# Performance work log

Measured on AMD Instinct MI355X. Metric: run time of the kernel, lower is better.

The kernel has to match this reference:

```python
import jax, jax.numpy as jnp
import numpy as np

B, T, C, H, K = 4, 2048, 1024, 16, 64
CHUNK = 64
NUM_LAYERS, LAYER_ID = 12, 6
D_MIX, D_DECAY = 32, 64


def setup_inputs() -> dict:
    key = jax.random.key(0)
    ks = jax.random.split(key, 12)
    x = jax.random.normal(ks[0], (B, T, C), jnp.float32)
    shift_state_in = jax.random.normal(ks[1], (B, C), jnp.float32)
    wkv_state_in = jnp.zeros((B, H, K, K), jnp.float32)

    r01 = LAYER_ID / max(NUM_LAYERS - 1, 1)
    r10 = 1.0 - LAYER_ID / NUM_LAYERS
    ddd = (np.arange(C, dtype=np.float64) / C)
    maa = lambda p: jnp.asarray((1.0 - ddd ** p).reshape(1, 1, C), jnp.float32)
    time_maa_x = maa(r10)
    time_maa_w = maa(r10)
    time_maa_k = maa(r10)
    time_maa_v = jnp.asarray((1.0 - (ddd ** r10 + 0.3 * r01)).reshape(1, 1, C), jnp.float32)
    time_maa_r = maa(0.5 * r10)
    time_maa_g = maa(0.5 * r10)
    time_maa_w1 = jax.random.uniform(ks[2], (C, D_MIX * 5), jnp.float32, -0.01, 0.01)
    time_maa_w2 = jax.random.uniform(ks[3], (5, D_MIX, C), jnp.float32, -0.01, 0.01)

    n = np.arange(C, dtype=np.float64)
    time_decay = jnp.asarray((-6 + 5 * (n / (C - 1)) ** (0.7 + 1.3 * r01)).reshape(1, 1, C), jnp.float32)
    time_decay_w1 = jax.random.uniform(ks[4], (C, D_DECAY), jnp.float32, -0.01, 0.01)
    time_decay_w2 = jax.random.uniform(ks[5], (D_DECAY, C), jnp.float32, -0.01, 0.01)

    zig = ((n + 1) % 3 - 1) * 0.1
    time_faaaa = jnp.asarray((r01 * (1 - n / (C - 1)) + zig).reshape(H, K), jnp.float32)
    lucid_temperature = jnp.ones((1, H, 1, 1), jnp.float32)

    s = 0.02
    W_r = jax.random.normal(ks[6], (C, C), jnp.float32) * s
    W_k = jax.random.normal(ks[7], (C, C), jnp.float32) * s
    W_v = jax.random.normal(ks[8], (C, C), jnp.float32) * s
    W_g = jax.random.normal(ks[9], (C, C), jnp.float32) * s
    W_o = jax.random.normal(ks[10], (C, C), jnp.float32) * s
    ln_gamma = jnp.ones((C,), jnp.float32)
    ln_beta = jnp.zeros((C,), jnp.float32)

    return dict(x=x, shift_state_in=shift_state_in, wkv_state_in=wkv_state_in,
                time_maa_x=time_maa_x, time_maa_w=time_maa_w, time_maa_k=time_maa_k,
                time_maa_v=time_maa_v, time_maa_r=time_maa_r, time_maa_g=time_maa_g,
                time_maa_w1=time_maa_w1, time_maa_w2=time_maa_w2,
                time_decay=time_decay, time_decay_w1=time_decay_w1, time_decay_w2=time_decay_w2,
                time_faaaa=time_faaaa, lucid_temperature=lucid_temperature,
                W_r=W_r, W_k=W_k, W_v=W_v, W_g=W_g, W_o=W_o,
                ln_gamma=ln_gamma, ln_beta=ln_beta)


def _forward(x, shift_state_in, wkv_state_in, time_maa_x, time_maa_w, time_maa_k,
             time_maa_v, time_maa_r, time_maa_g, time_maa_w1, time_maa_w2,
             time_decay, time_decay_w1, time_decay_w2, time_faaaa, lucid_temperature,
             W_r, W_k, W_v, W_g, W_o, ln_gamma, ln_beta):
    # ddlerp token shift
    dxprev = jnp.concatenate([shift_state_in[:, None, :], x[:, :-1]], axis=1) - x
    xxx = jnp.tanh((x + dxprev * time_maa_x) @ time_maa_w1).reshape(B, T, 5, D_MIX)
    m = jnp.einsum('btfd,fdc->fbtc', xxx, time_maa_w2)  # (5,B,T,C)
    mw, mk, mv, mr, mg = m[0], m[1], m[2], m[3], m[4]
    xw = x + dxprev * (time_maa_w + mw)
    xk = x + dxprev * (time_maa_k + mk)
    xv = x + dxprev * (time_maa_v + mv)
    xr = x + dxprev * (time_maa_r + mr)
    xg = x + dxprev * (time_maa_g + mg)

    r = xr @ W_r.T
    k = xk @ W_k.T
    v = xv @ W_v.T
    g = jax.nn.silu(xg @ W_g.T)
    w = time_decay + jnp.tanh(xw @ time_decay_w1) @ time_decay_w2

    tohead = lambda a: a.reshape(B, T, H, K).transpose(0, 2, 1, 3)  # (B,H,T,K)
    r_h, k_h, v_h = tohead(r), tohead(k), tohead(v)
    w_h = -jnp.exp(tohead(w))  # log-decay, negative
    u = time_faaaa.reshape(1, H, 1, K)
    temp = jax.nn.softplus(lucid_temperature)  # (1,H,1,1)

    n_chunks = T // CHUNK
    tochunks = lambda a: a.reshape(B, H, n_chunks, CHUNK, K).transpose(2, 0, 1, 3, 4)
    eye = jnp.eye(CHUNK, dtype=jnp.float32)
    mid = CHUNK // 2

    def step(state, inp):
        r_c, k_c, v_c, w_log = inp  # each (B,H,cs,K)
        w_cum = jnp.cumsum(w_log, axis=-2)
        w_shift = jnp.pad(w_cum[..., :-1, :], ((0, 0), (0, 0), (1, 0), (0, 0)))
        offset = w_shift[..., mid:mid + 1, :]
        r_decay = jnp.exp(jnp.clip(w_shift - offset, -30, 30))
        k_inv_decay = jnp.exp(jnp.clip(offset - w_cum, -30, 30))
        A = jnp.einsum('bhtk,bhsk->bhts', r_c * r_decay, k_c * k_inv_decay)
        A = jnp.tril(A, -1) + eye * jnp.sum(r_c * (u * k_c), axis=-1)[..., None]
        k_norm = k_c / jnp.maximum(jnp.linalg.norm(k_c, axis=-1, keepdims=True), 1e-12)
        K_gram = jnp.einsum('bhtk,bhsk->bhts', k_norm, k_norm)
        P = eye + jnp.exp(jnp.clip(temp * K_gram, -20, 20))
        P_v = jnp.linalg.solve(P, v_c)
        w_intra = jnp.exp(jnp.clip(w_cum - w_log, -30, 30))
        y = A @ P_v + (r_c * w_intra) @ state
        w_sum = jnp.sum(w_log, axis=-2, keepdims=True)  # (B,H,1,K)
        w_inter = jnp.exp(jnp.clip(w_sum - w_cum, -30, 30))
        new_state = state * jnp.exp(w_sum) + jnp.einsum('bhtk,bhtv->bhkv', k_c * w_inter, v_c)
        return new_state, y

    state_out, ys = jax.lax.scan(
        step, wkv_state_in,
        (tochunks(r_h), tochunks(k_h), tochunks(v_h), tochunks(w_h)))
    # (n,B,H,cs,K) -> (B,T,C)
    y = ys.transpose(1, 2, 0, 3, 4).reshape(B, H, T, K).transpose(0, 2, 1, 3).reshape(B, T, C)

    # GroupNorm with n_head groups, eps = 1e-5 * head_size_divisor**2
    eps = 1e-5 * 64.0
    yg = y.reshape(B, T, H, K)
    mu = yg.mean(axis=-1, keepdims=True)
    var = yg.var(axis=-1, keepdims=True)
    yn = (yg - mu) / jnp.sqrt(var + eps)
    yn = yn * ln_gamma.reshape(1, 1, H, K) + ln_beta.reshape(1, 1, H, K)
    yn = yn.reshape(B, T, C)

    out = (yn * g) @ W_o.T
    return out, x[:, -1], state_out


def reference(x, shift_state_in, wkv_state_in, time_maa_x, time_maa_w, time_maa_k,
              time_maa_v, time_maa_r, time_maa_g, time_maa_w1, time_maa_w2,
              time_decay, time_decay_w1, time_decay_w2, time_faaaa, lucid_temperature,
              W_r, W_k, W_v, W_g, W_o, ln_gamma, ln_beta):
    return _forward(x, shift_state_in, wkv_state_in, time_maa_x, time_maa_w, time_maa_k,
                    time_maa_v, time_maa_r, time_maa_g, time_maa_w1, time_maa_w2,
                    time_decay, time_decay_w1, time_decay_w2, time_faaaa, lucid_temperature,
                    W_r, W_k, W_v, W_g, W_o, ln_gamma, ln_beta)
```

## Files before the change

### kernel.cpp

```cpp
#include <hip/hip_runtime.h>
#include <cstdint>
#include <cstddef>

typedef unsigned short ushort_t;
#define DEVI __device__ __forceinline__

constexpr int Bc = 4, Tc = 2048, Cc = 1024, Hc = 16;
constexpr int BT = Bc * Tc;
constexpr int NCHUNK = Tc / 64;

using f32x4  = __attribute__((ext_vector_type(4))) float;
using bf16x8 = __attribute__((ext_vector_type(8))) __bf16;

DEVI ushort_t f2bf(float f) {
  union { float f; unsigned u; } v; v.f = f;
  unsigned r = v.u + 0x7fffu + ((v.u >> 16) & 1u);
  return (ushort_t)(r >> 16);
}
DEVI float bf2f(ushort_t u) {
  union { unsigned u; float f; } v; v.u = ((unsigned)u) << 16; return v.f;
}
DEVI float clip30(float x) { return fminf(fmaxf(x, -30.f), 30.f); }
DEVI float clip20(float x) { return fminf(fmaxf(x, -20.f), 20.f); }

DEVI float4 bf4up(uint2 r) {
  float4 v;
  v.x = bf2f((ushort_t)(r.x & 0xffff)); v.y = bf2f((ushort_t)(r.x >> 16));
  v.z = bf2f((ushort_t)(r.y & 0xffff)); v.w = bf2f((ushort_t)(r.y >> 16));
  return v;
}
DEVI uint2 f4pk(float4 v) {
  uint2 r;
  r.x = (unsigned)f2bf(v.x) | ((unsigned)f2bf(v.y) << 16);
  r.y = (unsigned)f2bf(v.z) | ((unsigned)f2bf(v.w) << 16);
  return r;
}

DEVI void gload_lds16(const ushort_t* g, ushort_t* l) {
  __builtin_amdgcn_global_load_lds(
      (const __attribute__((address_space(1))) void*)g,
      (__attribute__((address_space(3))) void*)l, 16, 0, 0);
}

#define GETEL(V4, E) ((E) == 0 ? (V4).x : (E) == 1 ? (V4).y : (E) == 2 ? (V4).z : (V4).w)
#define SETEL(V4, E, VAL) do { if ((E) == 0) (V4).x = (VAL); else if ((E) == 1) (V4).y = (VAL); \
                               else if ((E) == 2) (V4).z = (VAL); else (V4).w = (VAL); } while (0)

__global__ void k_f2bf5(const float* __restrict__ i0, const float* __restrict__ i1,
                        const float* __restrict__ i2, const float* __restrict__ i3,
                        const float* __restrict__ i4,
                        ushort_t* __restrict__ o0, ushort_t* __restrict__ o1,
                        ushort_t* __restrict__ o2, ushort_t* __restrict__ o3,
                        ushort_t* __restrict__ o4) {
  int z = blockIdx.z;
  const float* in = (z == 0) ? i0 : (z == 1) ? i1 : (z == 2) ? i2 : (z == 3) ? i3 : i4;
  ushort_t* out   = (z == 0) ? o0 : (z == 1) ? o1 : (z == 2) ? o2 : (z == 3) ? o3 : o4;
  int i = blockIdx.x * 256 + threadIdx.x;
  if (i < Cc * Cc / 4) {
    float4 v = *(const float4*)(in + (size_t)i * 4);
    ushort4 o;
    o.x = f2bf(v.x); o.y = f2bf(v.y); o.z = f2bf(v.z); o.w = f2bf(v.w);
    *(ushort4*)(out + (size_t)i * 4) = o;
  }
}

__global__ void k_prep(const float* __restrict__ w2, const float* __restrict__ w1,
                       const float* __restrict__ dw1, const float* __restrict__ x,
                       ushort_t* __restrict__ w2t, ushort_t* __restrict__ w1t,
                       ushort_t* __restrict__ dw1t, float* __restrict__ xlast) {
  int i = blockIdx.x * 256 + threadIdx.x;
  if (i < 163840) {
    int c = i / 160, fd = i % 160;
    w2t[i] = f2bf(w2[(size_t)fd * 1024 + c]);
  } else if (i < 327680) {
    int j = i - 163840; int n = j >> 10, r = j & 1023;
    w1t[j] = f2bf(w1[(size_t)r * 160 + n]);
  } else if (i < 393216) {
    int j = i - 327680; int n = j >> 10, r = j & 1023;
    dw1t[j] = f2bf(dw1[(size_t)r * 64 + n]);
  } else if (i < 397312) {
    int j = i - 393216; int b = j >> 10, c = j & 1023;
    xlast[j] = x[((size_t)b * Tc + Tc - 1) * Cc + c];
  }
}

__global__ __launch_bounds__(256) void k_shift_tanh(
    const float* __restrict__ x, const float* __restrict__ sst,
    const float* __restrict__ tmx, const ushort_t* __restrict__ Wt,
    ushort_t* __restrict__ outv) {
  constexpr int NCOLS = 160, NF = NCOLS / 16;
  int tid = threadIdx.x;
  int wave = tid >> 6, lane = tid & 63;
  int row0 = (blockIdx.x * 4 + wave) * 16;
  int lr = lane & 15, lk = (lane >> 4) * 8;
  int rg = row0 + lr;
  int tt = rg & (Tc - 1);
  const float* xrow = x + (size_t)rg * Cc;
  const float* prow = (tt == 0) ? (sst + (size_t)(rg >> 11) * Cc) : (xrow - Cc);
  f32x4 acc[NF];
  #pragma unroll
  for (int n = 0; n < NF; ++n) acc[n] = (f32x4){0.f, 0.f, 0.f, 0.f};
  for (int k0 = 0; k0 < 1024; k0 += 32) {
    int c0 = k0 + lk;
    float4 xa = *(const float4*)(xrow + c0), xb = *(const float4*)(xrow + c0 + 4);
    float4 pa = *(const float4*)(prow + c0), pb = *(const float4*)(prow + c0 + 4);
    float4 ta = *(const float4*)(tmx + c0), tb = *(const float4*)(tmx + c0 + 4);
    union { bf16x8 v; uint2 u[2]; } cv;
    cv.u[0] = f4pk(make_float4(xa.x + (pa.x - xa.x) * ta.x, xa.y + (pa.y - xa.y) * ta.y,
                               xa.z + (pa.z - xa.z) * ta.z, xa.w + (pa.w - xa.w) * ta.w));
    cv.u[1] = f4pk(make_float4(xb.x + (pb.x - xb.x) * tb.x, xb.y + (pb.y - xb.y) * tb.y,
                               xb.z + (pb.z - xb.z) * tb.z, xb.w + (pb.w - xb.w) * tb.w));
    #pragma unroll
    for (int n = 0; n < NF; ++n) {
      bf16x8 b = *(const bf16x8*)&Wt[(size_t)(n * 16 + lr) * 1024 + k0 + lk];
      acc[n] = __builtin_amdgcn_mfma_f32_16x16x32_bf16(cv.v, b, acc[n], 0, 0, 0);
    }
  }
  #pragma unroll
  for (int n = 0; n < NF; ++n) {
    #pragma unroll
    for (int q = 0; q < 4; ++q) {
      int row = row0 + (lane >> 4) * 4 + q;
      size_t oi = (size_t)row * NCOLS + n * 16 + lr;
      outv[oi] = f2bf(tanhf(acc[n][q]));
    }
  }
}

template<int NCOLS, int OBF>
__global__ __launch_bounds__(256) void k_tanh_mfma(const ushort_t* __restrict__ A,
                                                   const ushort_t* __restrict__ Wt,
                                                   void* __restrict__ outv) {
  constexpr int NF = NCOLS / 16;
  int tid = threadIdx.x;
  int wave = tid >> 6, lane = tid & 63;
  int row0 = (blockIdx.x * 4 + wave) * 16;
  int lr = lane & 15, lk = (lane >> 4) * 8;
  f32x4 acc[NF];
  #pragma unroll
  for (int n = 0; n < NF; ++n) acc[n] = (f32x4){0.f, 0.f, 0.f, 0.f};
  for (int k0 = 0; k0 < 1024; k0 += 32) {
    bf16x8 a = *(const bf16x8*)&A[(size_t)(row0 + lr) * 1024 + k0 + lk];
    #pragma unroll
    for (int n = 0; n < NF; ++n) {
      bf16x8 b = *(const bf16x8*)&Wt[(size_t)(n * 16 + lr) * 1024 + k0 + lk];
      acc[n] = __builtin_amdgcn_mfma_f32_16x16x32_bf16(a, b, acc[n], 0, 0, 0);
    }
  }
  #pragma unroll
  for (int n = 0; n < NF; ++n) {
    #pragma unroll
    for (int q = 0; q < 4; ++q) {
      int row = row0 + (lane >> 4) * 4 + q;
      size_t oi = (size_t)row * NCOLS + n * 16 + lr;
      float v = tanhf(acc[n][q]);
      if (OBF == 1) ((ushort_t*)outv)[oi] = f2bf(v);
      else          ((float*)outv)[oi] = v;
    }
  }
}

__global__ __launch_bounds__(256) void k_mix5m(
    const float* __restrict__ x, const float* __restrict__ sst,
    const ushort_t* __restrict__ t160b, const ushort_t* __restrict__ w2t,
    const float* __restrict__ maaw, const float* __restrict__ maak,
    const float* __restrict__ maav, const float* __restrict__ maar,
    const float* __restrict__ maag,
    ushort_t* __restrict__ xw, ushort_t* __restrict__ xk, ushort_t* __restrict__ xv,
    ushort_t* __restrict__ xr, ushort_t* __restrict__ xg) {
  __shared__ __align__(16) ushort_t As[64 * 168];
  __shared__ __align__(16) ushort_t Bs[64 * 168];
  int tid = threadIdx.x;
  int lane = tid & 63;
  int bRow = blockIdx.x * 64, bCol = blockIdx.y * 64;
  #pragma unroll
  for (int i = 0; i < 5; ++i) {
    int e = tid + i * 256;
    int r = e / 20, cc = (e % 20) * 8;
    *(int4*)&As[r * 168 + cc] = *(const int4*)&t160b[(size_t)(bRow + r) * 160 + cc];
    *(int4*)&Bs[r * 168 + cc] = *(const int4*)&w2t[(size_t)(bCol + r) * 160 + cc];
  }
  __syncthreads();
  int wm = tid >> 7, wn = (tid >> 6) & 1;
  f32x4 acc[5][2][2];
  #pragma unroll
  for (int f = 0; f < 5; ++f)
    #pragma unroll
    for (int m = 0; m < 2; ++m)
      #pragma unroll
      for (int n = 0; n < 2; ++n) acc[f][m][n] = (f32x4){0.f, 0.f, 0.f, 0.f};
  #pragma unroll
  for (int f = 0; f < 5; ++f) {
    bf16x8 af[2], bfv[2];
    #pragma unroll
    for (int m = 0; m < 2; ++m)
      af[m] = *(const bf16x8*)&As[(wm * 32 + m * 16 + (lane & 15)) * 168 + f * 32 + (lane >> 4) * 8];
    #pragma unroll
    for (int n = 0; n < 2; ++n)
      bfv[n] = *(const bf16x8*)&Bs[(wn * 32 + n * 16 + (lane & 15)) * 168 + f * 32 + (lane >> 4) * 8];
    #pragma unroll
    for (int m = 0; m < 2; ++m)
      #pragma unroll
      for (int n = 0; n < 2; ++n)
        acc[f][m][n] = __builtin_amdgcn_mfma_f32_16x16x32_bf16(af[m], bfv[n], acc[f][m][n], 0, 0, 0);
  }
  #pragma unroll
  for (int n = 0; n < 2; ++n) {
    int col = bCol + wn * 32 + n * 16 + (lane & 15);
    float mw_c = maaw[col], mk_c = maak[col], mv_c = maav[col];
    float mr_c = maar[col], mg_c = maag[col];
    #pragma unroll
    for (int m = 0; m < 2; ++m) {
      int row0 = bRow + wm * 32 + m * 16 + (lane >> 4) * 4;
      #pragma unroll
      for (int q = 0; q < 4; ++q) {
        int rg = row0 + q;
        int tt = rg & (Tc - 1);
        size_t g = (size_t)rg * Cc + col;
        float xv0 = x[g];
        float xprev = (tt == 0) ? sst[(size_t)(rg >> 11) * Cc + col] : x[g - Cc];
        float dv = xprev - xv0;
        xw[g] = f2bf(xv0 + dv * (mw_c + acc[0][m][n][q]));
        xk[g] = f2bf(xv0 + dv * (mk_c + acc[1][m][n][q]));
        xv[g] = f2bf(xv0 + dv * (mv_c + acc[2][m][n][q]));
        xr[g] = f2bf(xv0 + dv * (mr_c + acc[3][m][n][q]));
        xg[g] = f2bf(xv0 + dv * (mg_c + acc[4][m][n][q]));
      }
    }
  }
}

template<int EPI, int OBF>
DEVI void gemm_body(const ushort_t* __restrict__ A, const ushort_t* __restrict__ Wt,
                    void* __restrict__ outv, ushort_t* As, ushort_t* Bs,
                    int bRow, int bCol) {
  int tid = threadIdx.x;
  int wave = tid >> 6, lane = tid & 63;
  int wm = wave >> 1, wn = wave & 1;
  int lr = lane >> 2;
  int lkb = (((lane & 3) ^ ((lane >> 3) & 3))) * 8;
  int pch = ((lane >> 4) ^ ((lane >> 1) & 3)) * 8;
  f32x4 zero4 = {0.f, 0.f, 0.f, 0.f};
  f32x4 acc[4][4];
  #pragma unroll
  for (int m = 0; m < 4; ++m)
    #pragma unroll
    for (int n = 0; n < 4; ++n) acc[m][n] = zero4;

#define STAGEK(OFS, K0) do { \
    _Pragma("unroll") \
    for (int i = 0; i < 2; ++i) { \
      int row = (wave + 4 * i) * 16 + lr; \
      gload_lds16(A + (size_t)(bRow + row) * 1024 + (K0) + lkb, &As[(OFS) + (wave + 4 * i) * 512]); \
      gload_lds16(Wt + (size_t)(bCol + row) * 1024 + (K0) + lkb, &Bs[(OFS) + (wave + 4 * i) * 512]); \
    } } while (0)
#define CMP(OFS) do { \
    bf16x8 af[4], bfv[4]; \
    _Pragma("unroll") \
    for (int m = 0; m < 4; ++m) \
      af[m] = *(const bf16x8*)&As[(OFS) + (wm * 64 + m * 16 + (lane & 15)) * 32 + pch]; \
    _Pragma("unroll") \
    for (int n = 0; n < 4; ++n) \
      bfv[n] = *(const bf16x8*)&Bs[(OFS) + (wn * 64 + n * 16 + (lane & 15)) * 32 + pch]; \
    _Pragma("unroll") \
    for (int m = 0; m < 4; ++m) \
      _Pragma("unroll") \
      for (int n = 0; n < 4; ++n) \
        acc[m][n] = __builtin_amdgcn_mfma_f32_16x16x32_bf16(af[m], bfv[n], acc[m][n], 0, 0, 0); \
  } while (0)

  for (int k0 = 0; k0 < 1024; k0 += 64) {
    STAGEK(0, k0);
    STAGEK(4096, k0 + 32);
    __syncthreads();
    CMP(0);
    CMP(4096);
    __syncthreads();
  }
#undef STAGEK
#undef CMP

  #pragma unroll
  for (int m = 0; m < 4; ++m) {
    int row = bRow + wm * 64 + m * 16 + (lane >> 4) * 4;
    #pragma unroll
    for (int n = 0; n < 4; ++n) {
      int col = bCol + wn * 64 + n * 16 + (lane & 15);
      #pragma unroll
      for (int q = 0; q < 4; ++q) {
        float v = acc[m][n][q];
        if (EPI == 1) v = v / (1.f + __expf(-v));
        size_t oi = (size_t)(row + q) * 1024 + col;
        if (OBF == 1) ((ushort_t*)outv)[oi] = f2bf(v);
        else          ((float*)outv)[oi] = v;
      }
    }
  }
}

__global__ __launch_bounds__(256) void k_gemm4(
    const ushort_t* __restrict__ A0, const ushort_t* __restrict__ A1,
    const ushort_t* __restrict__ A2, const ushort_t* __restrict__ A3,
    const ushort_t* __restrict__ W0, const ushort_t* __restrict__ W1,
    const ushort_t* __restrict__ W2, const ushort_t* __restrict__ W3,
    ushort_t* __restrict__ O0, ushort_t* __restrict__ O1,
    ushort_t* __restrict__ O2, ushort_t* __restrict__ O3) {
  __shared__ __align__(16) ushort_t As[2 * 128 * 32];
  __shared__ __align__(16) ushort_t Bs[2 * 128 * 32];
  int z = blockIdx.z;
  const ushort_t* A  = (z == 0) ? A0 : (z == 1) ? A1 : (z == 2) ? A2 : A3;
  const ushort_t* Wt = (z == 0) ? W0 : (z == 1) ? W1 : (z == 2) ? W2 : W3;
  ushort_t* out      = (z == 0) ? O0 : (z == 1) ? O1 : (z == 2) ? O2 : O3;
  if (z == 3) gemm_body<1, 1>(A, Wt, out, As, Bs, blockIdx.x * 128, blockIdx.y * 128);
  else        gemm_body<0, 1>(A, Wt, out, As, Bs, blockIdx.x * 128, blockIdx.y * 128);
}

__global__ __launch_bounds__(256) void k_gemm_bm64(const ushort_t* __restrict__ A,
                                                   const ushort_t* __restrict__ Wt,
                                                   float* __restrict__ out) {
  __shared__ __align__(16) ushort_t As[2 * 64 * 32];
  __shared__ __align__(16) ushort_t Bs[2 * 128 * 32];
  int tid = threadIdx.x;
  int wave = tid >> 6, lane = tid & 63;
  int lr = lane >> 2;
  int lkb = (((lane & 3) ^ ((lane >> 3) & 3))) * 8;
  int pch = ((lane >> 4) ^ ((lane >> 1) & 3)) * 8;
  int bRow = blockIdx.x * 64, bCol = blockIdx.y * 128;
  f32x4 acc[4][2];
  #pragma unroll
  for (int m = 0; m < 4; ++m)
    #pragma unroll
    for (int n = 0; n < 2; ++n) acc[m][n] = (f32x4){0.f, 0.f, 0.f, 0.f};

#define STAGEK64(OA, OB, K0) do { \
    { int row = wave * 16 + lr; \
      gload_lds16(A + (size_t)(bRow + row) * 1024 + (K0) + lkb, &As[(OA) + wave * 512]); } \
    _Pragma("unroll") \
    for (int i = 0; i < 2; ++i) { \
      int row = (wave + 4 * i) * 16 + lr; \
      gload_lds16(Wt + (size_t)(bCol + row) * 1024 + (K0) + lkb, &Bs[(OB) + (wave + 4 * i) * 512]); \
    } } while (0)
#define CMP64(OA, OB) do { \
    bf16x8 af[4], bfv[2]; \
    _Pragma("unroll") \
    for (int m = 0; m < 4; ++m) \
      af[m] = *(const bf16x8*)&As[(OA) + (m * 16 + (lane & 15)) * 32 + pch]; \
    _Pragma("unroll") \
    for (int n = 0; n < 2; ++n) \
      bfv[n] = *(const bf16x8*)&Bs[(OB) + (wave * 32 + n * 16 + (lane & 15)) * 32 + pch]; \
    _Pragma("unroll") \
    for (int m = 0; m < 4; ++m) \
      _Pragma("unroll") \
      for (int n = 0; n < 2; ++n) \
        acc[m][n] = __builtin_amdgcn_mfma_f32_16x16x32_bf16(af[m], bfv[n], acc[m][n], 0, 0, 0); \
  } while (0)

  for (int k0 = 0; k0 < 1024; k0 += 64) {
    STAGEK64(0, 0, k0);
    STAGEK64(2048, 4096, k0 + 32);
    __syncthreads();
    CMP64(0, 0);
    CMP64(2048, 4096);
    __syncthreads();
  }
#undef STAGEK64
#undef CMP64

  #pragma unroll
  for (int m = 0; m < 4; ++m) {
    int row = bRow + m * 16 + (lane >> 4) * 4;
    #pragma unroll
    for (int n = 0; n < 2; ++n) {
      int col = bCol + wave * 32 + n * 16 + (lane & 15);
      #pragma unroll
      for (int q = 0; q < 4; ++q)
        out[(size_t)(row + q) * 1024 + col] = acc[m][n][q];
    }
  }
}

__global__ __launch_bounds__(256) void k_preA(
    const ushort_t* __restrict__ rbuf, const ushort_t* __restrict__ kbuf,
    const ushort_t* __restrict__ vbf,
    const ushort_t* __restrict__ t64bf, const float* __restrict__ dw2,
    const float* __restrict__ tdec, const float* __restrict__ faaaa,
    ushort_t* __restrict__ rwbf, ushort_t* __restrict__ kvbf, ushort_t* __restrict__ knbuf,
    ushort_t* __restrict__ Abf, float* __restrict__ esum) {
  __shared__ __align__(16) char ubuf[16640 + 9216 + 9216];
  float* wc = (float*)ubuf;
  ushort_t* sA = (ushort_t*)(ubuf + 16640);
  ushort_t* sB = (ushort_t*)(ubuf + 16640 + 9216);
  __shared__ float sred[4 * 64];
  __shared__ float sdiag[64];
  __shared__ float snrm[64];
  int bx = blockIdx.x;
  int ci = bx & 31, bh = bx >> 5;
  int b = bh >> 4, h = bh & 15;
  int tid = threadIdx.x;
  int w = tid >> 6, lane = tid & 63;
  int c = lane;
  int row0g = b * Tc + ci * 64;
  size_t base = (size_t)row0g * Cc + (size_t)h * 64;

  #pragma unroll
  for (int j = 0; j < 2; ++j) {
    int e = tid + j * 256; int r = e >> 3, cc = (e & 7) * 8;
    *(int4*)&sA[r * 72 + cc] = *(const int4*)&t64bf[(size_t)(row0g + r) * 64 + cc];
  }
  for (int i = 0; i < 16; ++i) {
    int e = tid + i * 256; int r = e >> 6, cc = e & 63;
    sB[cc * 72 + r] = f2bf(dw2[(size_t)r * Cc + h * 64 + cc]);
  }
  float rv[16], kv[16];
  #pragma unroll
  for (int i = 0; i < 16; ++i) {
    size_t g = base + (size_t)(w * 16 + i) * Cc + c;
    rv[i] = bf2f(rbuf[g]); kv[i] = bf2f(kbuf[g]);
  }
  __syncthreads();
  {
    int rbase = w * 16;
    bf16x8 a0 = *(const bf16x8*)&sA[(rbase + (lane & 15)) * 72 + (lane >> 4) * 8];
    bf16x8 a1 = *(const bf16x8*)&sA[(rbase + (lane & 15)) * 72 + 32 + (lane >> 4) * 8];
    #pragma unroll
    for (int ct = 0; ct < 4; ++ct) {
      bf16x8 b0 = *(const bf16x8*)&sB[(ct * 16 + (lane & 15)) * 72 + (lane >> 4) * 8];
      bf16x8 b1 = *(const bf16x8*)&sB[(ct * 16 + (lane & 15)) * 72 + 32 + (lane >> 4) * 8];
      f32x4 acc = {0.f, 0.f, 0.f, 0.f};
      acc = __builtin_amdgcn_mfma_f32_16x16x32_bf16(a0, b0, acc, 0, 0, 0);
      acc = __builtin_amdgcn_mfma_f32_16x16x32_bf16(a1, b1, acc, 0, 0, 0);
      int s = ct * 16 + (lane & 15);
      #pragma unroll
      for (int q = 0; q < 4; ++q) {
        int t = rbase + (lane >> 4) * 4 + q;
        wc[t * 65 + s] = acc[q];
      }
    }
  }
  __syncthreads();
  float wv[16];
  {
    float td = tdec[h * 64 + c];
    #pragma unroll
    for (int i = 0; i < 16; ++i)
      wv[i] = -__expf(td + wc[(w * 16 + i) * 65 + c]);
  }
  {
    float s = 0.f;
    #pragma unroll
    for (int i = 0; i < 16; ++i) s += wv[i];
    sred[w * 64 + c] = s;
  }
  __syncthreads();
  {
    float run = 0.f;
    for (int ww = 0; ww < w; ++ww) run += sred[ww * 64 + c];
    #pragma unroll
    for (int i = 0; i < 16; ++i) {
      run += wv[i]; wv[i] = run;
      wc[(w * 16 + i) * 65 + c] = run;
    }
    if (w == 3) esum[((size_t)bh * 32 + ci) * 64 + c] = __expf(run);
  }
  {
    float u_c = faaaa[h * 64 + c];
    #pragma unroll
    for (int i = 0; i < 16; ++i) {
      float p = rv[i] * kv[i] * u_c;
      float n2 = kv[i] * kv[i];
      #pragma unroll
      for (int o = 32; o; o >>= 1) { p += __shfl_xor(p, o, 64); n2 += __shfl_xor(n2, o, 64); }
      if (lane == 0) {
        sdiag[w * 16 + i] = p;
        snrm[w * 16 + i] = 1.f / fmaxf(sqrtf(n2), 1e-12f);
      }
    }
  }
  __syncthreads();
  float off32 = wc[31 * 65 + c];
  float wc63 = wc[63 * 65 + c];
  #pragma unroll
  for (int i = 0; i < 16; ++i) {
    int t = w * 16 + i;
    size_t g = base + (size_t)t * Cc + c;
    float wsh = (i == 0) ? ((w == 0) ? 0.f : wc[(t - 1) * 65 + c]) : wv[i - 1];
    rwbf[g] = f2bf(rv[i] * __expf(clip30(wsh)));
    sA[t * 72 + c] = f2bf(rv[i] * __expf(clip30(wsh - off32)));
    sB[t * 72 + c] = f2bf(kv[i] * __expf(clip30(off32 - wv[i])));
    knbuf[g] = f2bf(kv[i] * snrm[t]);
  }
  __syncthreads();
  {
    int rbase = w * 16;
    bf16x8 a0 = *(const bf16x8*)&sA[(rbase + (lane & 15)) * 72 + (lane >> 4) * 8];
    bf16x8 a1 = *(const bf16x8*)&sA[(rbase + (lane & 15)) * 72 + 32 + (lane >> 4) * 8];
    #pragma unroll
    for (int ct = 0; ct < 4; ++ct) {
      bf16x8 b0 = *(const bf16x8*)&sB[(ct * 16 + (lane & 15)) * 72 + (lane >> 4) * 8];
      bf16x8 b1 = *(const bf16x8*)&sB[(ct * 16 + (lane & 15)) * 72 + 32 + (lane >> 4) * 8];
      f32x4 acc = {0.f, 0.f, 0.f, 0.f};
      acc = __builtin_amdgcn_mfma_f32_16x16x32_bf16(a0, b0, acc, 0, 0, 0);
      acc = __builtin_amdgcn_mfma_f32_16x16x32_bf16(a1, b1, acc, 0, 0, 0);
      int s = ct * 16 + (lane & 15);
      #pragma unroll
      for (int q = 0; q < 4; ++q) {
        int t = rbase + (lane >> 4) * 4 + q;
        float val = (t > s) ? acc[q] : ((t == s) ? sdiag[t] : 0.f);
        Abf[(size_t)bx * 4096 + t * 64 + s] = f2bf(val);
      }
    }
  }
  __syncthreads();
  #pragma unroll
  for (int i = 0; i < 16; ++i) {
    int t = w * 16 + i;
    size_t g = base + (size_t)t * Cc + c;
    sA[c * 72 + t] = f2bf(kv[i] * __expf(clip30(wc63 - wv[i])));
    sB[c * 72 + t] = vbf[g];
  }
  __syncthreads();
  {
    int rbase = w * 16;
    bf16x8 a0 = *(const bf16x8*)&sA[(rbase + (lane & 15)) * 72 + (lane >> 4) * 8];
    bf16x8 a1 = *(const bf16x8*)&sA[(rbase + (lane & 15)) * 72 + 32 + (lane >> 4) * 8];
    #pragma unroll
    for (int ct = 0; ct < 4; ++ct) {
      bf16x8 b0 = *(const bf16x8*)&sB[(ct * 16 + (lane & 15)) * 72 + (lane >> 4) * 8];
      bf16x8 b1 = *(const bf16x8*)&sB[(ct * 16 + (lane & 15)) * 72 + 32 + (lane >> 4) * 8];
      f32x4 acc = {0.f, 0.f, 0.f, 0.f};
      acc = __builtin_amdgcn_mfma_f32_16x16x32_bf16(a0, b0, acc, 0, 0, 0);
      acc = __builtin_amdgcn_mfma_f32_16x16x32_bf16(a1, b1, acc, 0, 0, 0);
      int j = ct * 16 + (lane & 15);
      #pragma unroll
      for (int q = 0; q < 4; ++q) {
        int ii = rbase + (lane >> 4) * 4 + q;
        kvbf[base + (size_t)ii * Cc + j] = f2bf(acc[q]);
      }
    }
  }
}

__global__ __launch_bounds__(256) void k_preB(
    const ushort_t* __restrict__ knbuf, const ushort_t* __restrict__ vbf,
    const ushort_t* __restrict__ Abf, const ushort_t* __restrict__ rwbf,
    const ushort_t* __restrict__ statebuf, const float* __restrict__ ltemp,
    const ushort_t* __restrict__ gbuf, const float* __restrict__ gamma,
    const float* __restrict__ beta, ushort_t* __restrict__ ong) {
  __shared__ __align__(16) ushort_t sKX[64 * 72];
  __shared__ __align__(16) ushort_t sAb[64 * 72];
  __shared__ __align__(16) char ubuf[64 * 72 * 2 * 2];
  __shared__ __align__(16) float pivbuf[2][192];
  __shared__ float colbuf[2][64];
  __shared__ float diagbuf[64];
  float* sP = (float*)ubuf;
  ushort_t* sRW = (ushort_t*)ubuf;
  ushort_t* sSTt = (ushort_t*)(ubuf + 64 * 72 * 2);

  int bx = blockIdx.x;
  int ci = bx & 31, bh = bx >> 5;
  int b = bh >> 4, h = bh & 15;
  int tid = threadIdx.x;
  int w = tid >> 6, lane = tid & 63;
  int rg = tid >> 4, cg = tid & 15;
  size_t base = ((size_t)(b * Tc + ci * 64)) * Cc + (size_t)h * 64;

  #pragma unroll
  for (int j = 0; j < 2; ++j) {
    int e = tid + j * 256;
    int r = e >> 3, cc = (e & 7) * 8;
    *(int4*)&sKX[r * 72 + cc] = *(const int4*)&knbuf[base + (size_t)r * Cc + cc];
    *(int4*)&sAb[r * 72 + cc] = *(const int4*)&Abf[(size_t)bx * 4096 + (size_t)r * 64 + cc];
  }
  float4 A0, A1, A2, A3, B0, B1, B2, B3;
  if (cg >= 8) {
#define LDV(R, AR, BR) do { \
      int4 raw = *(const int4*)(vbf + base + (size_t)(4 * rg + (R)) * Cc + (cg - 8) * 8); \
      (AR).x = bf2f((ushort_t)(raw.x & 0xffff)); (AR).y = bf2f((ushort_t)((unsigned)raw.x >> 16)); \
      (AR).z = bf2f((ushort_t)(raw.y & 0xffff)); (AR).w = bf2f((ushort_t)((unsigned)raw.y >> 16)); \
      (BR).x = bf2f((ushort_t)(raw.z & 0xffff)); (BR).y = bf2f((ushort_t)((unsigned)raw.z >> 16)); \
      (BR).z = bf2f((ushort_t)(raw.w & 0xffff)); (BR).w = bf2f((ushort_t)((unsigned)raw.w >> 16)); \
    } while (0)
    LDV(0, A0, B0); LDV(1, A1, B1); LDV(2, A2, B2); LDV(3, A3, B3);
#undef LDV
  }
  __syncthreads();
  float temp = log1pf(__expf(ltemp[h]));
  {
    int rbase = w * 16;
    bf16x8 a0 = *(const bf16x8*)&sKX[(rbase + (lane & 15)) * 72 + (lane >> 4) * 8];
    bf16x8 a1 = *(const bf16x8*)&sKX[(rbase + (lane & 15)) * 72 + 32 + (lane >> 4) * 8];
    #pragma unroll
    for (int ct = 0; ct < 4; ++ct) {
      bf16x8 b0 = *(const bf16x8*)&sKX[(ct * 16 + (lane & 15)) * 72 + (lane >> 4) * 8];
      bf16x8 b1 = *(const bf16x8*)&sKX[(ct * 16 + (lane & 15)) * 72 + 32 + (lane >> 4) * 8];
      f32x4 acc = {0.f, 0.f, 0.f, 0.f};
      acc = __builtin_amdgcn_mfma_f32_16x16x32_bf16(a0, b0, acc, 0, 0, 0);
      acc = __builtin_amdgcn_mfma_f32_16x16x32_bf16(a1, b1, acc, 0, 0, 0);
      int s = ct * 16 + (lane & 15);
      #pragma unroll
      for (int q = 0; q < 4; ++q) {
        int t = rbase + (lane >> 4) * 4 + q;
        sP[t * 68 + s] = ((t == s) ? 1.f : 0.f) + __expf(clip20(temp * acc[q]));
      }
    }
  }
  __syncthreads();
  if (cg < 8) {
    A0 = *(float4*)&sP[(4 * rg + 0) * 68 + cg * 8]; B0 = *(float4*)&sP[(4 * rg + 0) * 68 + cg * 8 + 4];
    A1 = *(float4*)&sP[(4 * rg + 1) * 68 + cg * 8]; B1 = *(float4*)&sP[(4 * rg + 1) * 68 + cg * 8 + 4];
    A2 = *(float4*)&sP[(4 * rg + 2) * 68 + cg * 8]; B2 = *(float4*)&sP[(4 * rg + 2) * 68 + cg * 8 + 4];
    A3 = *(float4*)&sP[(4 * rg + 3) * 68 + cg * 8]; B3 = *(float4*)&sP[(4 * rg + 3) * 68 + cg * 8 + 4];
  }
  __syncthreads();
  #pragma unroll
  for (int j = 0; j < 2; ++j) {
    int e = tid + j * 256;
    int r = e >> 3, cc = (e & 7) * 8;
    *(int4*)&sRW[r * 72 + cc] = *(const int4*)&rwbf[base + (size_t)r * Cc + cc];
  }
  {
    const ushort_t* sb = statebuf + ((size_t)bh * 32 + ci) * 4096;
    #pragma unroll
    for (int i = 0; i < 16; ++i) {
      int e = tid + i * 256;
      int r = e >> 6, c = e & 63;
      sSTt[c * 72 + r] = sb[e];
    }
  }
#define UPD(MA, MB, F) do { \
    (MA).x -= (F) * p0_.x; (MA).y -= (F) * p0_.y; (MA).z -= (F) * p0_.z; (MA).w -= (F) * p0_.w; \
    (MB).x -= (F) * p1_.x; (MB).y -= (F) * p1_.y; (MB).z -= (F) * p1_.z; (MB).w -= (F) * p1_.w; \
  } while (0)
#define GJSTEP(JL, PRA, PRB, H0, H1, H2, H3) do { \
    int j_ = jh * 8 + (JL); \
    if (rg == (j_ >> 2)) { \
      *(float4*)&pivbuf[(JL) & 1][cg * 12]     = (PRA); \
      *(float4*)&pivbuf[(JL) & 1][cg * 12 + 4] = (PRB); \
    } \
    if (cg == jh) { \
      float4 cv_; \
      cv_.x = GETEL(H0, (JL) & 3); \
      cv_.y = GETEL(H1, (JL) & 3); \
      cv_.z = GETEL(H2, (JL) & 3); \
      cv_.w = GETEL(H3, (JL) & 3); \
      *(float4*)&colbuf[(JL) & 1][rg * 4] = cv_; \
    } \
    __syncthreads(); \
    float pd_ = pivbuf[(JL) & 1][(j_ >> 3) * 12 + (j_ & 7)]; \
    float4 fv_ = *(float4*)&colbuf[(JL) & 1][rg * 4]; \
    float4 p0_ = *(float4*)&pivbuf[(JL) & 1][cg * 12]; \
    float4 p1_ = *(float4*)&pivbuf[(JL) & 1][cg * 12 + 4]; \
    if (rg == (j_ >> 2)) SETEL(fv_, (JL) & 3, 0.f); \
    float inv_ = 1.f / pd_; \
    float f0_ = fv_.x * inv_, f1_ = fv_.y * inv_, f2_ = fv_.z * inv_, f3_ = fv_.w * inv_; \
    UPD(A0, B0, f0_); UPD(A1, B1, f1_); UPD(A2, B2, f2_); UPD(A3, B3, f3_); \
  } while (0)
  for (int jh = 0; jh < 8; ++jh) {
    GJSTEP(0, A0, B0, A0, A1, A2, A3);
    GJSTEP(1, A1, B1, A0, A1, A2, A3);
    GJSTEP(2, A2, B2, A0, A1, A2, A3);
    GJSTEP(3, A3, B3, A0, A1, A2, A3);
    GJSTEP(4, A0, B0, B0, B1, B2, B3);
    GJSTEP(5, A1, B1, B0, B1, B2, B3);
    GJSTEP(6, A2, B2, B0, B1, B2, B3);
    GJSTEP(7, A3, B3, B0, B1, B2, B3);
  }
#undef GJSTEP
#undef UPD
  if (cg == (rg >> 1)) {
    float4 h0 = (rg & 1) ? B0 : A0;
    float4 h1 = (rg & 1) ? B1 : A1;
    float4 h2 = (rg & 1) ? B2 : A2;
    float4 h3 = (rg & 1) ? B3 : A3;
    *(float4*)&diagbuf[rg * 4] = make_float4(h0.x, h1.y, h2.z, h3.w);
  }
  __syncthreads();
  if (cg >= 8) {
    float4 dg = *(float4*)&diagbuf[rg * 4];
#define WRX(R, AR, BR, IR) do { \
      int cb_ = (cg - 8) * 8; \
      sKX[(cb_ + 0) * 72 + 4 * rg + (R)] = f2bf((AR).x * (IR)); \
      sKX[(cb_ + 1) * 72 + 4 * rg + (R)] = f2bf((AR).y * (IR)); \
      sKX[(cb_ + 2) * 72 + 4 * rg + (R)] = f2bf((AR).z * (IR)); \
      sKX[(cb_ + 3) * 72 + 4 * rg + (R)] = f2bf((AR).w * (IR)); \
      sKX[(cb_ + 4) * 72 + 4 * rg + (R)] = f2bf((BR).x * (IR)); \
      sKX[(cb_ + 5) * 72 + 4 * rg + (R)] = f2bf((BR).y * (IR)); \
      sKX[(cb_ + 6) * 72 + 4 * rg + (R)] = f2bf((BR).z * (IR)); \
      sKX[(cb_ + 7) * 72 + 4 * rg + (R)] = f2bf((BR).w * (IR)); \
    } while (0)
    WRX(0, A0, B0, 1.f / dg.x);
    WRX(1, A1, B1, 1.f / dg.y);
    WRX(2, A2, B2, 1.f / dg.z);
    WRX(3, A3, B3, 1.f / dg.w);
#undef WRX
  }
  __syncthreads();
  {
    int rbase = w * 16;
    bf16x8 aA0 = *(const bf16x8*)&sAb[(rbase + (lane & 15)) * 72 + (lane >> 4) * 8];
    bf16x8 aA1 = *(const bf16x8*)&sAb[(rbase + (lane & 15)) * 72 + 32 + (lane >> 4) * 8];
    bf16x8 aR0 = *(const bf16x8*)&sRW[(rbase + (lane & 15)) * 72 + (lane >> 4) * 8];
    bf16x8 aR1 = *(const bf16x8*)&sRW[(rbase + (lane & 15)) * 72 + 32 + (lane >> 4) * 8];
    f32x4 yv[4];
    #pragma unroll
    for (int ct = 0; ct < 4; ++ct) {
      bf16x8 bX0 = *(const bf16x8*)&sKX[(ct * 16 + (lane & 15)) * 72 + (lane >> 4) * 8];
      bf16x8 bX1 = *(const bf16x8*)&sKX[(ct * 16 + (lane & 15)) * 72 + 32 + (lane >> 4) * 8];
      bf16x8 bS0 = *(const bf16x8*)&sSTt[(ct * 16 + (lane & 15)) * 72 + (lane >> 4) * 8];
      bf16x8 bS1 = *(const bf16x8*)&sSTt[(ct * 16 + (lane & 15)) * 72 + 32 + (lane >> 4) * 8];
      f32x4 acc = {0.f, 0.f, 0.f, 0.f};
      acc = __builtin_amdgcn_mfma_f32_16x16x32_bf16(aA0, bX0, acc, 0, 0, 0);
      acc = __builtin_amdgcn_mfma_f32_16x16x32_bf16(aA1, bX1, acc, 0, 0, 0);
      acc = __builtin_amdgcn_mfma_f32_16x16x32_bf16(aR0, bS0, acc, 0, 0, 0);
      acc = __builtin_amdgcn_mfma_f32_16x16x32_bf16(aR1, bS1, acc, 0, 0, 0);
      yv[ct] = acc;
    }
    #pragma unroll
    for (int q = 0; q < 4; ++q) {
      float s1 = yv[0][q] + yv[1][q] + yv[2][q] + yv[3][q];
      float s2 = yv[0][q] * yv[0][q] + yv[1][q] * yv[1][q] +
                 yv[2][q] * yv[2][q] + yv[3][q] * yv[3][q];
      #pragma unroll
      for (int o = 1; o < 16; o <<= 1) {
        s1 += __shfl_xor(s1, o, 64);
        s2 += __shfl_xor(s2, o, 64);
      }
      float mu = s1 * (1.f / 64.f);
      float var = s2 * (1.f / 64.f) - mu * mu;
      float rs = rsqrtf(var + 6.4e-4f);
      int t = rbase + (lane >> 4) * 4 + q;
      #pragma unroll
      for (int ct = 0; ct < 4; ++ct) {
        int cc = ct * 16 + (lane & 15);
        size_t g = base + (size_t)t * Cc + cc;
        float yn = (yv[ct][q] - mu) * rs;
        float o = (yn * gamma[h * 64 + cc] + beta[h * 64 + cc]) * bf2f(gbuf[g]);
        ong[g] = f2bf(o);
      }
    }
  }
}

__global__ __launch_bounds__(128) void k_scanstate(
    const float* __restrict__ wkv0, const ushort_t* __restrict__ kvbf,
    const float* __restrict__ esum, ushort_t* __restrict__ statebuf,
    float* __restrict__ stout) {
  int bh = blockIdx.x >> 3;
  int rg = blockIdx.x & 7;
  int b = bh >> 4, h = bh & 15;
  int tid = threadIdx.x;
  int r = rg * 8 + (tid >> 4);
  int c0 = (tid & 15) * 4;
  float4 st = *(const float4*)(wkv0 + ((size_t)bh * 64 + r) * 64 + c0);
  size_t kvb = (size_t)(b * Tc) * Cc + (size_t)h * 64 + (size_t)r * Cc + c0;
  constexpr int PF = 4;
  uint2 kvn[PF];
  float4 evn[PF];
  #pragma unroll
  for (int j = 0; j < PF; ++j) {
    kvn[j] = *(const uint2*)(kvbf + kvb + (size_t)j * 64 * Cc);
    evn[j] = *(const float4*)(esum + ((size_t)bh * 32 + j) * 64 + c0);
  }
  #pragma unroll
  for (int ci = 0; ci < NCHUNK; ++ci) {
    *(uint2*)(statebuf + ((size_t)bh * 32 + ci) * 4096 + (size_t)r * 64 + c0) = f4pk(st);
    float4 kv = bf4up(kvn[ci & 3]);
    float4 ev = evn[ci & 3];
    if (ci + PF < NCHUNK) {
      kvn[ci & 3] = *(const uint2*)(kvbf + kvb + (size_t)(ci + PF) * 64 * Cc);
      evn[ci & 3] = *(const float4*)(esum + ((size_t)bh * 32 + ci + PF) * 64 + c0);
    }
    st.x = st.x * ev.x + kv.x;
    st.y = st.y * ev.y + kv.y;
    st.z = st.z * ev.z + kv.z;
    st.w = st.w * ev.w + kv.w;
  }
  *(float4*)(stout + ((size_t)bh * 64 + r) * 64 + c0) = st;
}

extern "C" void kernel_launch(void* const* d_in, const int* in_sizes, int n_in,
                              void* d_out, int out_size, void* d_ws, size_t ws_size,
                              hipStream_t stream) {
  (void)in_sizes; (void)n_in; (void)out_size;
  const float* x     = (const float*)d_in[0];
  const float* sst   = (const float*)d_in[1];
  const float* wkv0  = (const float*)d_in[2];
  const float* tmx   = (const float*)d_in[3];
  const float* tmw   = (const float*)d_in[4];
  const float* tmk   = (const float*)d_in[5];
  const float* tmv   = (const float*)d_in[6];
  const float* tmr   = (const float*)d_in[7];
  const float* tmg   = (const float*)d_in[8];
  const float* w1    = (const float*)d_in[9];
  const float* w2    = (const float*)d_in[10];
  const float* tdec  = (const float*)d_in[11];
  const float* dw1   = (const float*)d_in[12];
  const float* dw2   = (const float*)d_in[13];
  const float* faaaa = (const float*)d_in[14];
  const float* ltemp = (const float*)d_in[15];
  const float* Wr    = (const float*)d_in[16];
  const float* Wk    = (const float*)d_in[17];
  const float* Wv    = (const float*)d_in[18];
  const float* Wg    = (const float*)d_in[19];
  const float* Wo    = (const float*)d_in[20];
  const float* lng   = (const float*)d_in[21];
  const float* lnb   = (const float*)d_in[22];
  float* out = (float*)d_out;

  const size_t MB = 1ull << 20;
  const size_t NEED = 242 * MB;
  if (ws_size < NEED) return;

  char* p = (char*)d_ws;
  ushort_t* kbb  = (ushort_t*)(p + 0 * MB);
  ushort_t* xwb  = (ushort_t*)(p + 16 * MB);
  ushort_t* rbb  = (ushort_t*)(p + 16 * MB);
  ushort_t* kvbf = (ushort_t*)(p + 32 * MB);
  ushort_t* statebuf = (ushort_t*)(p + 96 * MB);
  ushort_t* vbuf = (ushort_t*)(p + 128 * MB);
  ushort_t* gbuf = (ushort_t*)(p + 144 * MB);
  ushort_t* xkb  = (ushort_t*)(p + 160 * MB);
  ushort_t* Abf  = (ushort_t*)(p + 160 * MB);
  ushort_t* xvb  = (ushort_t*)(p + 176 * MB);
  ushort_t* rwbf = (ushort_t*)(p + 176 * MB);
  ushort_t* xrb  = (ushort_t*)(p + 192 * MB);
  ushort_t* xgb  = (ushort_t*)(p + 208 * MB);
  ushort_t* t160b = (ushort_t*)(p + 224 * MB);
  float*    esum = (float*)(p + 224 * MB);
  ushort_t* w2t  = (ushort_t*)(p + 227 * MB);
  ushort_t* w1t  = (ushort_t*)(p + 228 * MB);
  ushort_t* dw1t = (ushort_t*)(p + 229 * MB);
  ushort_t* t64bf = (ushort_t*)(p + 230 * MB);
  ushort_t* Wrb  = (ushort_t*)(p + 232 * MB);
  ushort_t* Wkb  = (ushort_t*)(p + 234 * MB);
  ushort_t* Wvb  = (ushort_t*)(p + 236 * MB);
  ushort_t* Wgb  = (ushort_t*)(p + 238 * MB);
  ushort_t* Wob  = (ushort_t*)(p + 240 * MB);

  const int thr = 256;
  k_f2bf5<<<dim3((Cc * Cc / 4 + 255) / 256, 1, 5), thr, 0, stream>>>(
      Wr, Wk, Wv, Wg, Wo, Wrb, Wkb, Wvb, Wgb, Wob);
  k_prep<<<(397312 + 255) / 256, thr, 0, stream>>>(w2, w1, dw1, x,
                                                   w2t, w1t, dw1t, out + (size_t)BT * Cc);

  k_shift_tanh<<<BT / 64, thr, 0, stream>>>(x, sst, tmx, w1t, t160b);
  k_mix5m<<<dim3(BT / 64, Cc / 64), thr, 0, stream>>>(x, sst, t160b, w2t,
                                                      tmw, tmk, tmv, tmr, tmg,
                                                      xwb, xkb, xvb, xrb, xgb);
  k_tanh_mfma<64, 1><<<BT / 64, thr, 0, stream>>>(xwb, dw1t, t64bf);

  k_gemm4<<<dim3(BT / 128, Cc / 128, 4), thr, 0, stream>>>(
      xrb, xkb, xvb, xgb, Wrb, Wkb, Wvb, Wgb, rbb, kbb, vbuf, gbuf);

  k_preA<<<2048, thr, 0, stream>>>(rbb, kbb, vbuf, t64bf, dw2, tdec, faaaa,
                                   rwbf, kvbf, xgb , Abf, esum);
  k_scanstate<<<512, 128, 0, stream>>>(wkv0, kvbf, esum, statebuf,
                                       out + (size_t)BT * Cc + (size_t)Bc * Cc);
  k_preB<<<2048, thr, 0, stream>>>(xgb , vbuf, Abf, rwbf, statebuf, ltemp,
                                   gbuf, lng, lnb, xgb );

  k_gemm_bm64<<<dim3(BT / 64, Cc / 128), thr, 0, stream>>>(xgb, Wob, out);
}
```

Before: 408.9 us.

## Rewrite fused r/k/v/g GEMM as 256x256 tile, 8-wave, double-buffered pipeline

Replaces the 128x128, 4-wave GEMM for the four input projections with a 256x256 tile computed by 8 waves. LDS is double-buffered for A and B, and async global-to-LDS loads for the next k-step are interleaved with MFMA quarters, using explicit barriers, waitcnt and setprio scheduling. The aim is more data reuse per loaded tile and load latency hidden behind compute. In exchange it uses larger register and LDS footprints and launches only 512 blocks, which may hurt occupancy and load balance across CUs.

```diff
diff --git a/kernel.cpp b/kernel.cpp
--- a/kernel.cpp
+++ b/kernel.cpp
@@ -230,89 +230,169 @@
   }
 }
 
-template<int EPI, int OBF>
-DEVI void gemm_body(const ushort_t* __restrict__ A, const ushort_t* __restrict__ Wt,
-                    void* __restrict__ outv, ushort_t* As, ushort_t* Bs,
-                    int bRow, int bCol) {
+template<int EPI>
+DEVI void gemm256_body(const ushort_t* __restrict__ A, const ushort_t* __restrict__ Wt,
+                       ushort_t* __restrict__ out,
+                       ushort_t* As0, ushort_t* As1, ushort_t* Bs0, ushort_t* Bs1) {
   int tid = threadIdx.x;
-  int wave = tid >> 6, lane = tid & 63;
-  int wm = wave >> 1, wn = wave & 1;
-  int lr = lane >> 2;
-  int lkb = (((lane & 3) ^ ((lane >> 3) & 3))) * 8;
+  int wid = tid >> 6, lane = tid & 63;
+  int wm = wid >> 2, wn = wid & 3;
+  int lr = lane & 15;
+  int bRow = blockIdx.x * 256, bCol = blockIdx.y * 256;
+  int lkb = ((lane & 3) ^ ((lane >> 3) & 3)) * 8;
   int pch = ((lane >> 4) ^ ((lane >> 1) & 3)) * 8;
-  f32x4 zero4 = {0.f, 0.f, 0.f, 0.f};
-  f32x4 acc[4][4];
-  #pragma unroll
-  for (int m = 0; m < 4; ++m)
-    #pragma unroll
-    for (int n = 0; n < 4; ++n) acc[m][n] = zero4;
-
-#define STAGEK(OFS, K0) do { \
+
+  f32x4 acc[8][4];
+  #pragma unroll
+  for (int m = 0; m < 8; ++m)
+    #pragma unroll
+    for (int n = 0; n < 4; ++n) acc[m][n] = (f32x4){0.f, 0.f, 0.f, 0.f};
+  bf16x8 a[4][2], b[2][2][2];
+
+#define STG_A(LB, t, h) do { \
     _Pragma("unroll") \
-    for (int i = 0; i < 2; ++i) { \
-      int row = (wave + 4 * i) * 16 + lr; \
-      gload_lds16(A + (size_t)(bRow + row) * 1024 + (K0) + lkb, &As[(OFS) + (wave + 4 * i) * 512]); \
-      gload_lds16(Wt + (size_t)(bCol + row) * 1024 + (K0) + lkb, &Bs[(OFS) + (wave + 4 * i) * 512]); \
+    for (int kh = 0; kh < 2; ++kh) \
+      gload_lds16(A + (size_t)(bRow + (h) * 128 + wid * 16 + (lane >> 2)) * 1024 \
+                    + (t) * 64 + kh * 32 + lkb, \
+                  (LB) + ((h) * 2 + kh) * 4096 + wid * 512 + lane * 8); \
+  } while (0)
+#define STG_B(LB, t, h) do { \
+    _Pragma("unroll") \
+    for (int kh = 0; kh < 2; ++kh) \
+      gload_lds16(Wt + (size_t)(bCol + (h) * 128 + wid * 16 + (lane >> 2)) * 1024 \
+                     + (t) * 64 + kh * 32 + lkb, \
+                  (LB) + ((h) * 2 + kh) * 4096 + wid * 512 + lane * 8); \
+  } while (0)
+#define LDAF(LB, mh) do { \
+    _Pragma("unroll") \
+    for (int m = 0; m < 4; ++m) { \
+      _Pragma("unroll") \
+      for (int kh = 0; kh < 2; ++kh) \
+        a[m][kh] = *(const bf16x8*)((LB) + (wm * 2 + kh) * 4096 \
+                                    + ((mh) * 4 + m) * 512 + lr * 32 + pch); \
     } } while (0)
-#define CMP(OFS) do { \
-    bf16x8 af[4], bfv[4]; \
+#define LDBF(LB, nh) do { \
     _Pragma("unroll") \
-    for (int m = 0; m < 4; ++m) \
-      af[m] = *(const bf16x8*)&As[(OFS) + (wm * 64 + m * 16 + (lane & 15)) * 32 + pch]; \
+    for (int n = 0; n < 2; ++n) { \
+      _Pragma("unroll") \
+      for (int kh = 0; kh < 2; ++kh) \
+        b[nh][n][kh] = *(const bf16x8*)((LB) + ((wn >> 1) * 2 + kh) * 4096 \
+                                        + (((wn & 1) * 4 + (nh) * 2 + n)) * 512 + lr * 32 + pch); \
+    } } while (0)
+#define MQ(mh, nh) do { \
     _Pragma("unroll") \
-    for (int n = 0; n < 4; ++n) \
-      bfv[n] = *(const bf16x8*)&Bs[(OFS) + (wn * 64 + n * 16 + (lane & 15)) * 32 + pch]; \
-    _Pragma("unroll") \
-    for (int m = 0; m < 4; ++m) \
+    for (int kk = 0; kk < 2; ++kk) \
       _Pragma("unroll") \
-      for (int n = 0; n < 4; ++n) \
-        acc[m][n] = __builtin_amdgcn_mfma_f32_16x16x32_bf16(af[m], bfv[n], acc[m][n], 0, 0, 0); \
+      for (int m = 0; m < 4; ++m) \
+        _Pragma("unroll") \
+        for (int n = 0; n < 2; ++n) \
+          acc[(mh) * 4 + m][(nh) * 2 + n] = __builtin_amdgcn_mfma_f32_16x16x32_bf16( \
+              a[m][kk], b[nh][n][kk], acc[(mh) * 4 + m][(nh) * 2 + n], 0, 0, 0); \
   } while (0)
-
-  for (int k0 = 0; k0 < 1024; k0 += 64) {
-    STAGEK(0, k0);
-    STAGEK(4096, k0 + 32);
-    __syncthreads();
-    CMP(0);
-    CMP(4096);
-    __syncthreads();
-  }
-#undef STAGEK
-#undef CMP
-
-  #pragma unroll
-  for (int m = 0; m < 4; ++m) {
-    int row = bRow + wm * 64 + m * 16 + (lane >> 4) * 4;
+#define SB0() __builtin_amdgcn_sched_barrier(0)
+#define MID(mh, nh) do { \
+    __builtin_amdgcn_s_barrier(); \
+    asm volatile("s_waitcnt lgkmcnt(0)" ::: "memory"); \
+    SB0(); \
+    __builtin_amdgcn_s_setprio(1); \
+    MQ(mh, nh); \
+    SB0(); \
+    __builtin_amdgcn_s_setprio(0); \
+  } while (0)
+#define ENDP() do { __builtin_amdgcn_s_barrier(); SB0(); } while (0)
+#define VMW(N) asm volatile("s_waitcnt vmcnt(" #N ")" ::: "memory")
+
+  STG_A(As0, 0, 0); STG_A(As0, 0, 1);
+  STG_B(Bs0, 0, 0); STG_B(Bs0, 0, 1);
+  STG_B(Bs1, 1, 0); STG_B(Bs1, 1, 1);
+  VMW(4);
+  __builtin_amdgcn_s_barrier();
+  SB0();
+
+  #pragma unroll 1
+  for (int it = 0; it < 7; ++it) {
+    int t1 = it * 2 + 1, t2 = it * 2 + 2, t3 = it * 2 + 3;
+    LDAF(As0, 0); LDBF(Bs0, 0); SB0();
+    STG_A(As1, t1, 0);
+    MID(0, 0); ENDP();
+    LDBF(Bs0, 1); SB0();
+    STG_A(As1, t1, 1);
+    MID(0, 1); ENDP();
+    LDAF(As0, 1); SB0();
+    STG_B(Bs0, t2, 0);
+    MID(1, 0); ENDP();
+    STG_B(Bs0, t2, 1);
+    MID(1, 1); VMW(4); ENDP();
+    LDAF(As1, 0); LDBF(Bs1, 0); SB0();
+    STG_A(As0, t2, 0);
+    MID(0, 0); ENDP();
+    LDBF(Bs1, 1); SB0();
+    STG_A(As0, t2, 1);
+    MID(0, 1); ENDP();
+    LDAF(As1, 1); SB0();
+    STG_B(Bs1, t3, 0);
+    MID(1, 0); ENDP();
+    STG_B(Bs1, t3, 1);
+    MID(1, 1); VMW(4); ENDP();
+  }
+  LDAF(As0, 0); LDBF(Bs0, 0); SB0();
+  STG_A(As1, 15, 0);
+  MID(0, 0); ENDP();
+  LDBF(Bs0, 1); SB0();
+  STG_A(As1, 15, 1);
+  MID(0, 1); ENDP();
+  LDAF(As0, 1); SB0();
+  MID(1, 0); ENDP();
+  MID(1, 1); VMW(0); ENDP();
+  LDAF(As1, 0); LDBF(Bs1, 0); SB0();
+  MID(0, 0); ENDP();
+  LDBF(Bs1, 1); SB0();
+  MID(0, 1); ENDP();
+  LDAF(As1, 1); SB0();
+  MID(1, 0); ENDP();
+  MID(1, 1);
+
+#undef STG_A
+#undef STG_B
+#undef LDAF
+#undef LDBF
+#undef MQ
+#undef SB0
+#undef MID
+#undef ENDP
+#undef VMW
+
+  #pragma unroll
+  for (int m = 0; m < 8; ++m) {
+    int row = bRow + wm * 128 + m * 16 + (lane >> 4) * 4;
     #pragma unroll
     for (int n = 0; n < 4; ++n) {
-      int col = bCol + wn * 64 + n * 16 + (lane & 15);
+      int col = bCol + wn * 64 + n * 16 + lr;
       #pragma unroll
       for (int q = 0; q < 4; ++q) {
         float v = acc[m][n][q];
         if (EPI == 1) v = v / (1.f + __expf(-v));
-        size_t oi = (size_t)(row + q) * 1024 + col;
-        if (OBF == 1) ((ushort_t*)outv)[oi] = f2bf(v);
-        else          ((float*)outv)[oi] = v;
+        out[(size_t)(row + q) * 1024 + col] = f2bf(v);
       }
     }
   }
 }
 
-__global__ __launch_bounds__(256) void k_gemm4(
+__global__ __launch_bounds__(512, 2) void k_gemm4x(
     const ushort_t* __restrict__ A0, const ushort_t* __restrict__ A1,
     const ushort_t* __restrict__ A2, const ushort_t* __restrict__ A3,
     const ushort_t* __restrict__ W0, const ushort_t* __restrict__ W1,
     const ushort_t* __restrict__ W2, const ushort_t* __restrict__ W3,
     ushort_t* __restrict__ O0, ushort_t* __restrict__ O1,
     ushort_t* __restrict__ O2, ushort_t* __restrict__ O3) {
-  __shared__ __align__(16) ushort_t As[2 * 128 * 32];
-  __shared__ __align__(16) ushort_t Bs[2 * 128 * 32];
+  __shared__ __align__(16) ushort_t As[2][16384];
+  __shared__ __align__(16) ushort_t Bs[2][16384];
   int z = blockIdx.z;
   const ushort_t* A  = (z == 0) ? A0 : (z == 1) ? A1 : (z == 2) ? A2 : A3;
   const ushort_t* Wt = (z == 0) ? W0 : (z == 1) ? W1 : (z == 2) ? W2 : W3;
   ushort_t* out      = (z == 0) ? O0 : (z == 1) ? O1 : (z == 2) ? O2 : O3;
-  if (z == 3) gemm_body<1, 1>(A, Wt, out, As, Bs, blockIdx.x * 128, blockIdx.y * 128);
-  else        gemm_body<0, 1>(A, Wt, out, As, Bs, blockIdx.x * 128, blockIdx.y * 128);
+  if (z == 3) gemm256_body<1>(A, Wt, out, As[0], As[1], Bs[0], Bs[1]);
+  else        gemm256_body<0>(A, Wt, out, As[0], As[1], Bs[0], Bs[1]);
 }
 
 __global__ __launch_bounds__(256) void k_gemm_bm64(const ushort_t* __restrict__ A,
@@ -849,7 +929,7 @@
                                                       xwb, xkb, xvb, xrb, xgb);
   k_tanh_mfma<64, 1><<<BT / 64, thr, 0, stream>>>(xwb, dw1t, t64bf);
 
-  k_gemm4<<<dim3(BT / 128, Cc / 128, 4), thr, 0, stream>>>(
+  k_gemm4x<<<dim3(BT / 256, Cc / 256, 4), 512, 0, stream>>>(
       xrb, xkb, xvb, xgb, Wrb, Wkb, Wvb, Wgb, rbb, kbb, vbuf, gbuf);
 
   k_preA<<<2048, thr, 0, stream>>>(rbb, kbb, vbuf, t64bf, dw2, tdec, faaaa,
```

New measurement: 425.2 us. +4.0%, slower.
